# Performance work log

Hardware: AMD Instinct MI355X
Metric: run time of the kernel (lower is better)

The kernel has to match this reference:

```python
import jax, jax.numpy as jnp
import numpy as np

D_MODEL = 1024
N_HEADS = 16
D_K = D_MODEL // N_HEADS


def setup_inputs() -> dict:
    key = jax.random.key(0)
    ks = jax.random.split(key, 7)
    B, S = 2, 2048
    q = jax.random.normal(ks[0], (B, S, D_MODEL), dtype=jnp.float32)
    k = jax.random.normal(ks[1], (B, S, D_MODEL), dtype=jnp.float32)
    v = jax.random.normal(ks[2], (B, S, D_MODEL), dtype=jnp.float32)
    mask = jnp.ones((B, 1, S, S), dtype=bool)
    scale = 1.0 / np.sqrt(D_MODEL)
    w_q = jax.random.normal(ks[3], (D_MODEL, D_MODEL), dtype=jnp.float32) * scale
    w_k = jax.random.normal(ks[4], (D_MODEL, D_MODEL), dtype=jnp.float32) * scale
    w_v = jax.random.normal(ks[5], (D_MODEL, D_MODEL), dtype=jnp.float32) * scale
    w_o = jax.random.normal(ks[6], (D_MODEL, D_MODEL), dtype=jnp.float32) * scale
    return {"q": q, "k": k, "v": v, "mask": mask,
            "w_q": w_q, "w_k": w_k, "w_v": w_v, "w_o": w_o}


def reference(q, k, v, mask, w_q, w_k, w_v, w_o):
    B, S, _ = q.shape
    # projections (nn.Linear: x @ W^T, no bias)
    def split_heads(x):  # [B,S,D] -> [B,H,S,d_k]
        return x.reshape(B, -1, N_HEADS, D_K).transpose(0, 2, 1, 3)
    query = split_heads(q @ w_q.T)
    key_h = split_heads(k @ w_k.T)
    value = split_heads(v @ w_v.T)
    # naive scaled dot-product attention: full [B,H,S,S] scores materialized
    scores = jnp.einsum('bhqd,bhkd->bhqk', query, key_h) / jnp.sqrt(
        jnp.asarray(D_K, query.dtype))
    scores = jnp.where(mask, scores, jnp.asarray(-1e9, scores.dtype))
    attn = jax.nn.softmax(scores, axis=-1)  # dropout p=0.0 -> identity
    x = jnp.einsum('bhqk,bhkd->bhqd', attn, value)
    x = x.transpose(0, 2, 1, 3).reshape(B, S, N_HEADS * D_K)
    return x @ w_o.T
```

## Files before the change

kernel.cpp:

```cpp
#include <hip/hip_runtime.h>
#include <hip/hip_bf16.h>
#include <math.h>

typedef __bf16 bf16;
typedef __bf16 bf16x8 __attribute__((ext_vector_type(8)));
typedef float f32x4 __attribute__((ext_vector_type(4)));
typedef float f32x16 __attribute__((ext_vector_type(16)));
typedef unsigned u32x4 __attribute__((ext_vector_type(4)));

#define MFMA16(a, b, c) __builtin_amdgcn_mfma_f32_16x16x32_bf16((a), (b), (c), 0, 0, 0)
#define MFMA32(a, b, c) __builtin_amdgcn_mfma_f32_32x32x16_bf16((a), (b), (c), 0, 0, 0)

__device__ __forceinline__ void gl_lds16(const void* g, void* l) {
    __builtin_amdgcn_global_load_lds(
        (__attribute__((address_space(1))) void*)(g),
        (__attribute__((address_space(3))) void*)(l),
        16, 0, 0);
}

__device__ __forceinline__ unsigned cvt_pk_bf16(float lo, float hi) {
    unsigned r;
    asm("v_cvt_pk_bf16_f32 %0, %1, %2" : "=v"(r) : "v"(lo), "v"(hi));
    return r;
}

__global__ __launch_bounds__(256) void cvt7(
    const float* __restrict__ w0, const float* __restrict__ w1,
    const float* __restrict__ w2, const float* __restrict__ w3,
    const float* __restrict__ x0, const float* __restrict__ x1,
    const float* __restrict__ x2, bf16* __restrict__ dst) {
    const int z = blockIdx.y;
    const float* src;
    bf16* out;
    if (z < 4) {
        if (blockIdx.x >= 512) return;
        src = (z == 0) ? w0 : (z == 1) ? w1 : (z == 2) ? w2 : w3;
        out = dst + (size_t)z * 1048576;
    } else {
        src = (z == 4) ? x0 : (z == 5) ? x1 : x2;
        out = dst + 4 * 1048576 + (size_t)(z - 4) * 4194304;
    }
    const int i = (blockIdx.x * 256 + threadIdx.x) * 8;
    float4 a = ((const float4*)(src + i))[0];
    float4 b = ((const float4*)(src + i))[1];
    bf16x8 o;
    o[0] = (bf16)a.x; o[1] = (bf16)a.y; o[2] = (bf16)a.z; o[3] = (bf16)a.w;
    o[4] = (bf16)b.x; o[5] = (bf16)b.y; o[6] = (bf16)b.z; o[7] = (bf16)b.w;
    *(bf16x8*)(out + i) = o;
}

template <int EP>
__device__ __forceinline__ void gemm_bf(const bf16* __restrict__ A,
                                        const bf16* __restrict__ B,
                                        void* __restrict__ Cv,
                                        const int m0, const int n0) {
    constexpr int K = 1024;
    __shared__ __align__(16) bf16 As[128 * 64];
    __shared__ __align__(16) bf16 Bs[128 * 64];

    const int t = threadIdx.x;
    const int lane = t & 63;
    const int w = t >> 6;
    const int wm = (w & 1) * 64;
    const int wn = (w >> 1) * 64;
    const int lr = lane & 15;
    const int lq8 = (lane >> 4) * 8;
    const int rq = (lane >> 4) * 4;

    f32x4 acc[4][4] = {};

    const int srow = t >> 3;
    const int sch = (t & 7) * 8;
    char* lA = (char*)As;
    char* lB = (char*)Bs;

    for (int k0 = 0; k0 < K; k0 += 64) {
#pragma unroll
        for (int i = 0; i < 4; ++i) {
            gl_lds16(A + (size_t)(m0 + i * 32 + srow) * K + k0 + sch, lA + i * 4096 + t * 16);
            gl_lds16(B + (size_t)(n0 + i * 32 + srow) * K + k0 + sch, lB + i * 4096 + t * 16);
        }
        __syncthreads();

#pragma unroll
        for (int kk = 0; kk < 64; kk += 32) {
            bf16x8 af[4], bfr[4];
#pragma unroll
            for (int i = 0; i < 4; ++i) {
                af[i]  = *(const bf16x8*)&As[(wm + i * 16 + lr) * 64 + kk + lq8];
                bfr[i] = *(const bf16x8*)&Bs[(wn + i * 16 + lr) * 64 + kk + lq8];
            }
#pragma unroll
            for (int mi = 0; mi < 4; ++mi)
#pragma unroll
                for (int ni = 0; ni < 4; ++ni)
                    acc[mi][ni] = MFMA16(af[mi], bfr[ni], acc[mi][ni]);
        }
        __syncthreads();
    }

#pragma unroll
    for (int mi = 0; mi < 4; ++mi) {
#pragma unroll
        for (int ni = 0; ni < 4; ++ni) {
#pragma unroll
            for (int r = 0; r < 4; ++r) {
                const int m = m0 + wm + mi * 16 + rq + r;
                const int n = n0 + wn + ni * 16 + lr;
                const float vv = acc[mi][ni][r];
                if constexpr (EP == 0) {
                    bf16* C = (bf16*)Cv;
                    const int b = m >> 11, s = m & 2047;
                    const int h = n >> 6,  d = n & 63;
                    C[(((size_t)(b * 16 + h)) * 2048 + s) * 64 + d] = (bf16)vv;
                } else if constexpr (EP == 1) {
                    float* C = (float*)Cv;
                    C[(size_t)m * 1024 + n] = vv;
                } else {
                    bf16* C = (bf16*)Cv;
                    C[((size_t)(n >> 11) * 1024 + m) * 2048 + (n & 2047)] = (bf16)vv;
                }
            }
        }
    }
}

__global__ __launch_bounds__(256, 3) void qkv_bf(
    const bf16* __restrict__ Xq, const bf16* __restrict__ Xk,
    const bf16* __restrict__ Xv, const bf16* __restrict__ Wc,
    bf16* __restrict__ Qb, bf16* __restrict__ Kb, bf16* __restrict__ Vb) {
    const int z = blockIdx.z;
    if (z == 0)
        gemm_bf<0>(Xq, Wc, Qb, blockIdx.x * 128, blockIdx.y * 128);
    else if (z == 1)
        gemm_bf<0>(Xk, Wc + 1048576, Kb, blockIdx.x * 128, blockIdx.y * 128);
    else
        gemm_bf<2>(Wc + 2 * 1048576, Xv, Vb, blockIdx.y * 128, blockIdx.x * 128);
}

__global__ __launch_bounds__(512, 2) void out_gemm(
    const bf16* __restrict__ X, const bf16* __restrict__ W, float* __restrict__ C) {
    constexpr int K = 1024;
    __shared__ __align__(16) bf16 As[128 * 64];
    __shared__ __align__(16) bf16 Bs[128 * 64];

    const int t = threadIdx.x;
    const int lane = t & 63;
    const int w = t >> 6;
    const int wm = (w >> 2) * 64;
    const int wn = (w & 3) * 32;
    const int lr = lane & 15;
    const int lq8 = (lane >> 4) * 8;
    const int rq = (lane >> 4) * 4;
    const int m0 = blockIdx.x * 128, n0 = blockIdx.y * 128;

    f32x4 acc[4][2] = {};

    const int srow = t >> 3;
    const int sch = (t & 7) * 8;
    char* lA = (char*)As;
    char* lB = (char*)Bs;

    for (int k0 = 0; k0 < K; k0 += 64) {
#pragma unroll
        for (int i = 0; i < 2; ++i) {
            gl_lds16(X + (size_t)(m0 + i * 64 + srow) * K + k0 + sch, lA + i * 8192 + t * 16);
            gl_lds16(W + (size_t)(n0 + i * 64 + srow) * K + k0 + sch, lB + i * 8192 + t * 16);
        }
        __syncthreads();

#pragma unroll
        for (int kk = 0; kk < 64; kk += 32) {
            bf16x8 af[4], bfr[2];
#pragma unroll
            for (int i = 0; i < 4; ++i)
                af[i] = *(const bf16x8*)&As[(wm + i * 16 + lr) * 64 + kk + lq8];
#pragma unroll
            for (int i = 0; i < 2; ++i)
                bfr[i] = *(const bf16x8*)&Bs[(wn + i * 16 + lr) * 64 + kk + lq8];
#pragma unroll
            for (int mi = 0; mi < 4; ++mi)
#pragma unroll
                for (int ni = 0; ni < 2; ++ni)
                    acc[mi][ni] = MFMA16(af[mi], bfr[ni], acc[mi][ni]);
        }
        __syncthreads();
    }

#pragma unroll
    for (int mi = 0; mi < 4; ++mi)
#pragma unroll
        for (int ni = 0; ni < 2; ++ni)
#pragma unroll
            for (int r = 0; r < 4; ++r) {
                const int m = m0 + wm + mi * 16 + rq + r;
                const int n = n0 + wn + ni * 16 + lr;
                C[(size_t)m * 1024 + n] = acc[mi][ni][r];
            }
}

template <int MODE>
__device__ __forceinline__ void gemm_f32tok(const void* __restrict__ Av,
                                            const void* __restrict__ Bv,
                                            bf16* __restrict__ C,
                                            const int m0, const int n0) {
    constexpr int K = 1024;
    __shared__ __align__(16) bf16 As[128 * 32];
    __shared__ __align__(16) bf16 Bs[128 * 32];

    const int t = threadIdx.x;
    const int lane = t & 63;
    const int w = t >> 6;
    const int wm = (w & 1) * 64;
    const int wn = (w >> 1) * 64;
    const int lr = lane & 15;
    const int lq8 = (lane >> 4) * 8;
    const int rq = (lane >> 4) * 4;

    f32x4 acc[4][4] = {};
    const int srow = t >> 2;
    const int sch = (t & 3) * 8;
    const int ar = t >> 1;
    const int ac = (t & 1) * 16;
    char* lA = (char*)As;
    char* lB = (char*)Bs;

    for (int k0 = 0; k0 < K; k0 += 32) {
        if constexpr (MODE == 0) {
            const float* X = (const float*)Av;
            const float* p = X + (size_t)(m0 + ar) * K + k0 + ac;
            float4 f0 = ((const float4*)p)[0], f1 = ((const float4*)p)[1];
            float4 f2 = ((const float4*)p)[2], f3 = ((const float4*)p)[3];
            bf16x8 o0, o1;
            o0[0]=(bf16)f0.x; o0[1]=(bf16)f0.y; o0[2]=(bf16)f0.z; o0[3]=(bf16)f0.w;
            o0[4]=(bf16)f1.x; o0[5]=(bf16)f1.y; o0[6]=(bf16)f1.z; o0[7]=(bf16)f1.w;
            o1[0]=(bf16)f2.x; o1[1]=(bf16)f2.y; o1[2]=(bf16)f2.z; o1[3]=(bf16)f2.w;
            o1[4]=(bf16)f3.x; o1[5]=(bf16)f3.y; o1[6]=(bf16)f3.z; o1[7]=(bf16)f3.w;
            *(bf16x8*)&As[ar * 32 + ac]     = o0;
            *(bf16x8*)&As[ar * 32 + ac + 8] = o1;
        } else {
            const bf16* X = (const bf16*)Av;
            gl_lds16(X + (size_t)(m0 + srow) * K + k0 + sch,      lA + t * 16);
            gl_lds16(X + (size_t)(m0 + 64 + srow) * K + k0 + sch, lA + 4096 + t * 16);
        }
        if constexpr (MODE == 2) {
            const float* X = (const float*)Bv;
            const float* p = X + (size_t)(n0 + ar) * K + k0 + ac;
            float4 f0 = ((const float4*)p)[0], f1 = ((const float4*)p)[1];
            float4 f2 = ((const float4*)p)[2], f3 = ((const float4*)p)[3];
            bf16x8 o0, o1;
            o0[0]=(bf16)f0.x; o0[1]=(bf16)f0.y; o0[2]=(bf16)f0.z; o0[3]=(bf16)f0.w;
            o0[4]=(bf16)f1.x; o0[5]=(bf16)f1.y; o0[6]=(bf16)f1.z; o0[7]=(bf16)f1.w;
            o1[0]=(bf16)f2.x; o1[1]=(bf16)f2.y; o1[2]=(bf16)f2.z; o1[3]=(bf16)f2.w;
            o1[4]=(bf16)f3.x; o1[5]=(bf16)f3.y; o1[6]=(bf16)f3.z; o1[7]=(bf16)f3.w;
            *(bf16x8*)&Bs[ar * 32 + ac]     = o0;
            *(bf16x8*)&Bs[ar * 32 + ac + 8] = o1;
        } else {
            const bf16* W = (const bf16*)Bv;
            gl_lds16(W + (size_t)(n0 + srow) * K + k0 + sch,      lB + t * 16);
            gl_lds16(W + (size_t)(n0 + 64 + srow) * K + k0 + sch, lB + 4096 + t * 16);
        }
        __syncthreads();

        bf16x8 af[4], bfr[4];
#pragma unroll
        for (int i = 0; i < 4; ++i) {
            af[i]  = *(const bf16x8*)&As[(wm + i * 16 + lr) * 32 + lq8];
            bfr[i] = *(const bf16x8*)&Bs[(wn + i * 16 + lr) * 32 + lq8];
        }
#pragma unroll
        for (int mi = 0; mi < 4; ++mi)
#pragma unroll
            for (int ni = 0; ni < 4; ++ni)
                acc[mi][ni] = MFMA16(af[mi], bfr[ni], acc[mi][ni]);
        __syncthreads();
    }

#pragma unroll
    for (int mi = 0; mi < 4; ++mi) {
#pragma unroll
        for (int ni = 0; ni < 4; ++ni) {
#pragma unroll
            for (int r = 0; r < 4; ++r) {
                const int m = m0 + wm + mi * 16 + rq + r;
                const int n = n0 + wn + ni * 16 + lr;
                const float vv = acc[mi][ni][r];
                if constexpr (MODE == 0) {
                    const int b = m >> 11, s = m & 2047;
                    const int h = n >> 6,  d = n & 63;
                    C[(((size_t)(b * 16 + h)) * 2048 + s) * 64 + d] = (bf16)vv;
                } else {
                    C[((size_t)(n >> 11) * 1024 + m) * 2048 + (n & 2047)] = (bf16)vv;
                }
            }
        }
    }
}

__global__ __launch_bounds__(256, 2) void qkv_f32(
    const float* __restrict__ q, const float* __restrict__ k, const float* __restrict__ v,
    const bf16* __restrict__ Wc, bf16* __restrict__ Qb, bf16* __restrict__ Kb,
    bf16* __restrict__ Vb) {
    const int z = blockIdx.z;
    if (z == 0)
        gemm_f32tok<0>(q, Wc, Qb, blockIdx.x * 128, blockIdx.y * 128);
    else if (z == 1)
        gemm_f32tok<0>(k, Wc + 1048576, Kb, blockIdx.x * 128, blockIdx.y * 128);
    else
        gemm_f32tok<2>(Wc + 2 * 1048576, v, Vb, blockIdx.y * 128, blockIdx.x * 128);
}

__global__ __launch_bounds__(512, 4) void attn_kernel(
    const bf16* __restrict__ Qb, const bf16* __restrict__ Kb,
    const bf16* __restrict__ Vb, bf16* __restrict__ Xb) {
    constexpr int S = 2048;

    __shared__ __align__(16) bf16 smem[17408];

    const int t = threadIdx.x;
    const int lane = t & 63;
    const int w = t >> 6;
    const int wg = w & 3;
    const int kh = w >> 2;
    const int l31 = lane & 31;
    const int half = lane >> 5;

    const int lin = blockIdx.x;
    const int g = lin >> 3;
    const int bh = (lin & 7) + 8 * (g & 3);
    const int q0 = (g >> 2) * 128 + wg * 32;

    const bf16* Q  = Qb + (size_t)bh * S * 64;
    const bf16* Kh = Kb + (size_t)bh * S * 64;
    const bf16* Vh = Vb + (size_t)bh * 64 * S;

    const float qscale = 0.125f * 1.4426950408889634f;
    bf16x8 qf[4];
#pragma unroll
    for (int c = 0; c < 4; ++c) {
        bf16x8 v0 = *(const bf16x8*)(Q + (size_t)(q0 + l31) * 64 + c * 16 + half * 8);
#pragma unroll
        for (int e = 0; e < 8; ++e) v0[e] = (bf16)((float)v0[e] * qscale);
        qf[c] = v0;
    }

    f32x16 od[2] = {};
    float ls0 = 0.f, ls1 = 0.f, ls2 = 0.f, ls3 = 0.f;

    const int tt = t & 255;
    const int sr = tt >> 2;
    const int sc = (tt & 3) * 2;
    const bf16* pKg = Kh + ((size_t)kh * 1024 + sr) * 64 + sc * 8;
    const bf16* pVg = Vh + (size_t)sr * S + kh * 1024 + sc * 8;
    bf16* KsH = smem + kh * 4096;
    bf16* VsH = smem + 8192 + kh * 4096;
    int wKo[2];
#pragma unroll
    for (int c = 0; c < 2; ++c)
        wKo[c] = (sr >> 1) * 128 + ((((sr & 1) << 3) + sc + c) ^ ((sr >> 1) & 15)) * 8;

    bf16x8 pk[2], pv[2];
#pragma unroll
    for (int c = 0; c < 2; ++c) {
        pk[c] = *(const bf16x8*)(pKg + c * 8);
        pv[c] = *(const bf16x8*)(pVg + c * 8);
    }

    const int fbase = (l31 >> 1) * 128;
    const int fb8 = (l31 & 1) << 3;
    const int fsw = l31 >> 1;

    for (int j = 0; j < 16; ++j) {
        __syncthreads();
#pragma unroll
        for (int c = 0; c < 2; ++c) {
            *(bf16x8*)&KsH[wKo[c]] = pk[c];
            *(bf16x8*)&VsH[wKo[c]] = pv[c];
        }
        __syncthreads();

        f32x16 sacc[2] = {};
        __builtin_amdgcn_s_setprio(1);
#pragma unroll
        for (int kt = 0; kt < 2; ++kt) {
#pragma unroll
            for (int c = 0; c < 4; ++c) {
                bf16x8 kf = *(const bf16x8*)
                    &KsH[kt * 2048 + fbase + ((fb8 + c * 2 + half) ^ fsw) * 8];
                sacc[kt] = MFMA32(kf, qf[c], sacc[kt]);
            }
        }
        __builtin_amdgcn_s_setprio(0);

        if (j + 1 < 16) {
            pKg += 4096;
            pVg += 64;
#pragma unroll
            for (int c = 0; c < 2; ++c) {
                pk[c] = *(const bf16x8*)(pKg + c * 8);
                pv[c] = *(const bf16x8*)(pVg + c * 8);
            }
        }

#pragma unroll
        for (int kt = 0; kt < 2; ++kt) {
            float ex[16];
#pragma unroll
            for (int r = 0; r < 16; ++r)
                ex[r] = exp2f(sacc[kt][r]);
            ls0 += ex[0] + ex[4] + ex[8]  + ex[12];
            ls1 += ex[1] + ex[5] + ex[9]  + ex[13];
            ls2 += ex[2] + ex[6] + ex[10] + ex[14];
            ls3 += ex[3] + ex[7] + ex[11] + ex[15];

            unsigned pa[8];
#pragma unroll
            for (int c2 = 0; c2 < 2; ++c2) {
#pragma unroll
                for (int wd = 0; wd < 2; ++wd) {
                    unsigned x = cvt_pk_bf16(ex[c2 * 8 + wd * 2 + 0], ex[c2 * 8 + wd * 2 + 1]);
                    unsigned y = cvt_pk_bf16(ex[c2 * 8 + wd * 2 + 4], ex[c2 * 8 + wd * 2 + 5]);
                    asm("v_permlane32_swap_b32 %0, %1" : "+v"(x), "+v"(y));
                    pa[c2 * 4 + wd]     = x;
                    pa[c2 * 4 + wd + 2] = y;
                }
            }

            __builtin_amdgcn_s_setprio(1);
#pragma unroll
            for (int c2 = 0; c2 < 2; ++c2) {
                u32x4 aw;
                aw[0] = pa[c2 * 4 + 0]; aw[1] = pa[c2 * 4 + 1];
                aw[2] = pa[c2 * 4 + 2]; aw[3] = pa[c2 * 4 + 3];
                bf16x8 ap = __builtin_bit_cast(bf16x8, aw);
#pragma unroll
                for (int dt = 0; dt < 2; ++dt) {
                    const int cgv = kt * 4 + c2 * 2 + half;
                    bf16x8 vf = *(const bf16x8*)
                        &VsH[dt * 2048 + fbase + ((fb8 + cgv) ^ fsw) * 8];
                    od[dt] = MFMA32(ap, vf, od[dt]);
                }
            }
            __builtin_amdgcn_s_setprio(0);
        }
    }

    float lsum = ls0 + ls1 + ls2 + ls3;
    float ltot = lsum + __shfl_xor(lsum, 32);

    __syncthreads();
    float* fsm = (float*)smem;
    const int so = (wg * 64 + lane) * 34;
    if (kh == 1) {
        fsm[so + 32] = ltot;
#pragma unroll
        for (int r = 0; r < 16; ++r) {
            fsm[so + r]      = od[0][r];
            fsm[so + 16 + r] = od[1][r];
        }
    }
    __syncthreads();
    if (kh == 0) {
        ltot += fsm[so + 32];
        const float inv = 1.f / fmaxf(ltot, 1e-30f);
        const int b = bh >> 4, hh = bh & 15;
#pragma unroll
        for (int r = 0; r < 16; ++r) {
            const int qrow = (r & 3) + 8 * (r >> 2) + 4 * half;
            const float invr = __shfl(inv, qrow);
            const size_t base = ((size_t)(b * 2048 + q0 + qrow)) * 1024 + hh * 64;
            Xb[base + l31]      = (bf16)((od[0][r] + fsm[so + r]) * invr);
            Xb[base + 32 + l31] = (bf16)((od[1][r] + fsm[so + 16 + r]) * invr);
        }
    }
}

extern "C" void kernel_launch(void* const* d_in, const int* in_sizes, int n_in,
                              void* d_out, int out_size, void* d_ws, size_t ws_size,
                              hipStream_t stream) {
    const float* q  = (const float*)d_in[0];
    const float* k  = (const float*)d_in[1];
    const float* v  = (const float*)d_in[2];
    const float* wq = (const float*)d_in[4];
    const float* wk = (const float*)d_in[5];
    const float* wv = (const float*)d_in[6];
    const float* wo = (const float*)d_in[7];
    float* out = (float*)d_out;

    const bool big = ws_size >= (size_t)64 * 1024 * 1024;
    bf16* Wc = (bf16*)d_ws;
    const dim3 blk(256);

    if (big) {
        bf16* Xq = Wc + 4 * 1048576;
        bf16* Xk = Xq + 4194304;
        bf16* Xv = Xk + 4194304;
        bf16* Qb = Xv + 4194304;
        bf16* Kb = Qb + 4194304;
        bf16* Vb = Kb + 4194304;
        bf16* Xb = Vb + 4194304;
        cvt7<<<dim3(2048, 7), blk, 0, stream>>>(wq, wk, wv, wo, q, k, v, Wc);
        qkv_bf<<<dim3(32, 8, 3), blk, 0, stream>>>(Xq, Xk, Xv, Wc, Qb, Kb, Vb);
        attn_kernel<<<dim3(512), dim3(512), 0, stream>>>(Qb, Kb, Vb, Xb);
        out_gemm<<<dim3(32, 8), dim3(512), 0, stream>>>(Xb, Wc + 3 * 1048576, out);
    } else {
        bf16* Qb = Wc + 4 * 1048576;
        bf16* Kb = Qb + 4194304;
        bf16* Vb = Kb + 4194304;
        bf16* Xb = Vb + 4194304;
        cvt7<<<dim3(512, 4), blk, 0, stream>>>(wq, wk, wv, wo, q, k, v, Wc);
        qkv_f32<<<dim3(32, 8, 3), blk, 0, stream>>>(q, k, v, Wc, Qb, Kb, Vb);
        attn_kernel<<<dim3(512), dim3(512), 0, stream>>>(Qb, Kb, Vb, Xb);
        out_gemm<<<dim3(32, 8), dim3(512), 0, stream>>>(Xb, Wc + 3 * 1048576, out);
    }
}
```

Baseline: 267.6 us.

## Swizzle GEMM LDS tiles and give each attention wave two query tiles

The bf16 GEMM kernels now XOR-swizzle the 16-byte chunk index when staging tiles into LDS and when reading fragments, to avoid LDS bank conflicts on the MFMA operand loads. The attention kernel drops from 512 to 256 threads per block, with each wave handling 64 query rows (two 32-row tiles). Each K/V fragment read from LDS is therefore reused for two MFMAs, and each thread stages twice as many K/V chunks. The global prefetch of the next K/V tile now starts before the QK MFMAs, and the s_setprio hints are removed. This raises register pressure and halves waves per block, which can reduce latency hiding.

```diff
diff --git a/kernel.cpp b/kernel.cpp
--- a/kernel.cpp
+++ b/kernel.cpp
@@ -64,21 +64,22 @@
     const int wm = (w & 1) * 64;
     const int wn = (w >> 1) * 64;
     const int lr = lane & 15;
-    const int lq8 = (lane >> 4) * 8;
     const int rq = (lane >> 4) * 4;
+    const int ch0 = lane >> 4;
+    const int lsw = lr & 7;
 
     f32x4 acc[4][4] = {};
 
     const int srow = t >> 3;
-    const int sch = (t & 7) * 8;
+    const int scg = ((t & 7) ^ (srow & 7)) * 8;
     char* lA = (char*)As;
     char* lB = (char*)Bs;
 
     for (int k0 = 0; k0 < K; k0 += 64) {
 #pragma unroll
         for (int i = 0; i < 4; ++i) {
-            gl_lds16(A + (size_t)(m0 + i * 32 + srow) * K + k0 + sch, lA + i * 4096 + t * 16);
-            gl_lds16(B + (size_t)(n0 + i * 32 + srow) * K + k0 + sch, lB + i * 4096 + t * 16);
+            gl_lds16(A + (size_t)(m0 + i * 32 + srow) * K + k0 + scg, lA + i * 4096 + t * 16);
+            gl_lds16(B + (size_t)(n0 + i * 32 + srow) * K + k0 + scg, lB + i * 4096 + t * 16);
         }
         __syncthreads();
 
@@ -87,8 +88,10 @@
             bf16x8 af[4], bfr[4];
 #pragma unroll
             for (int i = 0; i < 4; ++i) {
-                af[i]  = *(const bf16x8*)&As[(wm + i * 16 + lr) * 64 + kk + lq8];
-                bfr[i] = *(const bf16x8*)&Bs[(wn + i * 16 + lr) * 64 + kk + lq8];
+                const int ro = (wm + i * 16 + lr) * 64 + ((((kk >> 3) + ch0) ^ lsw) * 8);
+                const int co = (wn + i * 16 + lr) * 64 + ((((kk >> 3) + ch0) ^ lsw) * 8);
+                af[i]  = *(const bf16x8*)&As[ro];
+                bfr[i] = *(const bf16x8*)&Bs[co];
             }
 #pragma unroll
             for (int mi = 0; mi < 4; ++mi)
@@ -150,22 +153,23 @@
     const int wm = (w >> 2) * 64;
     const int wn = (w & 3) * 32;
     const int lr = lane & 15;
-    const int lq8 = (lane >> 4) * 8;
     const int rq = (lane >> 4) * 4;
+    const int ch0 = lane >> 4;
+    const int lsw = lr & 7;
     const int m0 = blockIdx.x * 128, n0 = blockIdx.y * 128;
 
     f32x4 acc[4][2] = {};
 
     const int srow = t >> 3;
-    const int sch = (t & 7) * 8;
+    const int scg = ((t & 7) ^ (srow & 7)) * 8;
     char* lA = (char*)As;
     char* lB = (char*)Bs;
 
     for (int k0 = 0; k0 < K; k0 += 64) {
 #pragma unroll
         for (int i = 0; i < 2; ++i) {
-            gl_lds16(X + (size_t)(m0 + i * 64 + srow) * K + k0 + sch, lA + i * 8192 + t * 16);
-            gl_lds16(W + (size_t)(n0 + i * 64 + srow) * K + k0 + sch, lB + i * 8192 + t * 16);
+            gl_lds16(X + (size_t)(m0 + i * 64 + srow) * K + k0 + scg, lA + i * 8192 + t * 16);
+            gl_lds16(W + (size_t)(n0 + i * 64 + srow) * K + k0 + scg, lB + i * 8192 + t * 16);
         }
         __syncthreads();
 
@@ -174,10 +178,10 @@
             bf16x8 af[4], bfr[2];
 #pragma unroll
             for (int i = 0; i < 4; ++i)
-                af[i] = *(const bf16x8*)&As[(wm + i * 16 + lr) * 64 + kk + lq8];
+                af[i] = *(const bf16x8*)&As[(wm + i * 16 + lr) * 64 + ((((kk >> 3) + ch0) ^ lsw) * 8)];
 #pragma unroll
             for (int i = 0; i < 2; ++i)
-                bfr[i] = *(const bf16x8*)&Bs[(wn + i * 16 + lr) * 64 + kk + lq8];
+                bfr[i] = *(const bf16x8*)&Bs[(wn + i * 16 + lr) * 64 + ((((kk >> 3) + ch0) ^ lsw) * 8)];
 #pragma unroll
             for (int mi = 0; mi < 4; ++mi)
 #pragma unroll
@@ -310,7 +314,7 @@
         gemm_f32tok<2>(Wc + 2 * 1048576, v, Vb, blockIdx.y * 128, blockIdx.x * 128);
 }
 
-__global__ __launch_bounds__(512, 4) void attn_kernel(
+__global__ __launch_bounds__(256, 2) void attn_kernel(
     const bf16* __restrict__ Qb, const bf16* __restrict__ Kb,
     const bf16* __restrict__ Vb, bf16* __restrict__ Xb) {
     constexpr int S = 2048;
@@ -320,48 +324,53 @@
     const int t = threadIdx.x;
     const int lane = t & 63;
     const int w = t >> 6;
-    const int wg = w & 3;
-    const int kh = w >> 2;
+    const int wg = w & 1;
+    const int kh = w >> 1;
     const int l31 = lane & 31;
     const int half = lane >> 5;
 
     const int lin = blockIdx.x;
     const int g = lin >> 3;
     const int bh = (lin & 7) + 8 * (g & 3);
-    const int q0 = (g >> 2) * 128 + wg * 32;
+    const int q0 = (g >> 2) * 128 + wg * 64;
 
     const bf16* Q  = Qb + (size_t)bh * S * 64;
     const bf16* Kh = Kb + (size_t)bh * S * 64;
     const bf16* Vh = Vb + (size_t)bh * 64 * S;
 
     const float qscale = 0.125f * 1.4426950408889634f;
-    bf16x8 qf[4];
+    bf16x8 qfA[4], qfB[4];
 #pragma unroll
     for (int c = 0; c < 4; ++c) {
         bf16x8 v0 = *(const bf16x8*)(Q + (size_t)(q0 + l31) * 64 + c * 16 + half * 8);
-#pragma unroll
-        for (int e = 0; e < 8; ++e) v0[e] = (bf16)((float)v0[e] * qscale);
-        qf[c] = v0;
-    }
-
-    f32x16 od[2] = {};
-    float ls0 = 0.f, ls1 = 0.f, ls2 = 0.f, ls3 = 0.f;
-
-    const int tt = t & 255;
-    const int sr = tt >> 2;
-    const int sc = (tt & 3) * 2;
-    const bf16* pKg = Kh + ((size_t)kh * 1024 + sr) * 64 + sc * 8;
-    const bf16* pVg = Vh + (size_t)sr * S + kh * 1024 + sc * 8;
+        bf16x8 v1 = *(const bf16x8*)(Q + (size_t)(q0 + 32 + l31) * 64 + c * 16 + half * 8);
+#pragma unroll
+        for (int e = 0; e < 8; ++e) {
+            v0[e] = (bf16)((float)v0[e] * qscale);
+            v1[e] = (bf16)((float)v1[e] * qscale);
+        }
+        qfA[c] = v0;
+        qfB[c] = v1;
+    }
+
+    f32x16 odA[2] = {}, odB[2] = {};
+    float lsA0 = 0.f, lsA1 = 0.f, lsB0 = 0.f, lsB1 = 0.f;
+
+    const int tt = t & 127;
+    const int sr = tt >> 1;
+    const int scb = (tt & 1) * 4;
+    const bf16* pKg = Kh + ((size_t)kh * 1024 + sr) * 64 + scb * 8;
+    const bf16* pVg = Vh + (size_t)sr * S + kh * 1024 + scb * 8;
     bf16* KsH = smem + kh * 4096;
     bf16* VsH = smem + 8192 + kh * 4096;
-    int wKo[2];
-#pragma unroll
-    for (int c = 0; c < 2; ++c)
-        wKo[c] = (sr >> 1) * 128 + ((((sr & 1) << 3) + sc + c) ^ ((sr >> 1) & 15)) * 8;
-
-    bf16x8 pk[2], pv[2];
-#pragma unroll
-    for (int c = 0; c < 2; ++c) {
+    int wKo[4];
+#pragma unroll
+    for (int c = 0; c < 4; ++c)
+        wKo[c] = (sr >> 1) * 128 + ((((sr & 1) << 3) + scb + c) ^ ((sr >> 1) & 15)) * 8;
+
+    bf16x8 pk[4], pv[4];
+#pragma unroll
+    for (int c = 0; c < 4; ++c) {
         pk[c] = *(const bf16x8*)(pKg + c * 8);
         pv[c] = *(const bf16x8*)(pVg + c * 8);
     }
@@ -373,104 +382,120 @@
     for (int j = 0; j < 16; ++j) {
         __syncthreads();
 #pragma unroll
-        for (int c = 0; c < 2; ++c) {
+        for (int c = 0; c < 4; ++c) {
             *(bf16x8*)&KsH[wKo[c]] = pk[c];
             *(bf16x8*)&VsH[wKo[c]] = pv[c];
         }
         __syncthreads();
 
-        f32x16 sacc[2] = {};
-        __builtin_amdgcn_s_setprio(1);
+        if (j + 1 < 16) {
+            pKg += 4096;
+            pVg += 64;
+#pragma unroll
+            for (int c = 0; c < 4; ++c) {
+                pk[c] = *(const bf16x8*)(pKg + c * 8);
+                pv[c] = *(const bf16x8*)(pVg + c * 8);
+            }
+        }
+
 #pragma unroll
         for (int kt = 0; kt < 2; ++kt) {
+            f32x16 sA = {}, sB = {};
 #pragma unroll
             for (int c = 0; c < 4; ++c) {
                 bf16x8 kf = *(const bf16x8*)
                     &KsH[kt * 2048 + fbase + ((fb8 + c * 2 + half) ^ fsw) * 8];
-                sacc[kt] = MFMA32(kf, qf[c], sacc[kt]);
-            }
-        }
-        __builtin_amdgcn_s_setprio(0);
-
-        if (j + 1 < 16) {
-            pKg += 4096;
-            pVg += 64;
-#pragma unroll
-            for (int c = 0; c < 2; ++c) {
-                pk[c] = *(const bf16x8*)(pKg + c * 8);
-                pv[c] = *(const bf16x8*)(pVg + c * 8);
-            }
-        }
-
-#pragma unroll
-        for (int kt = 0; kt < 2; ++kt) {
-            float ex[16];
-#pragma unroll
-            for (int r = 0; r < 16; ++r)
-                ex[r] = exp2f(sacc[kt][r]);
-            ls0 += ex[0] + ex[4] + ex[8]  + ex[12];
-            ls1 += ex[1] + ex[5] + ex[9]  + ex[13];
-            ls2 += ex[2] + ex[6] + ex[10] + ex[14];
-            ls3 += ex[3] + ex[7] + ex[11] + ex[15];
-
-            unsigned pa[8];
+                sA = MFMA32(kf, qfA[c], sA);
+                sB = MFMA32(kf, qfB[c], sB);
+            }
+
+            float exA[16], exB[16];
+#pragma unroll
+            for (int r = 0; r < 16; ++r) {
+                exA[r] = exp2f(sA[r]);
+                exB[r] = exp2f(sB[r]);
+            }
+            lsA0 += exA[0] + exA[4] + exA[8]  + exA[12] + exA[2] + exA[6] + exA[10] + exA[14];
+            lsA1 += exA[1] + exA[5] + exA[9]  + exA[13] + exA[3] + exA[7] + exA[11] + exA[15];
+            lsB0 += exB[0] + exB[4] + exB[8]  + exB[12] + exB[2] + exB[6] + exB[10] + exB[14];
+            lsB1 += exB[1] + exB[5] + exB[9]  + exB[13] + exB[3] + exB[7] + exB[11] + exB[15];
+
+            unsigned paA[8], paB[8];
 #pragma unroll
             for (int c2 = 0; c2 < 2; ++c2) {
 #pragma unroll
                 for (int wd = 0; wd < 2; ++wd) {
-                    unsigned x = cvt_pk_bf16(ex[c2 * 8 + wd * 2 + 0], ex[c2 * 8 + wd * 2 + 1]);
-                    unsigned y = cvt_pk_bf16(ex[c2 * 8 + wd * 2 + 4], ex[c2 * 8 + wd * 2 + 5]);
-                    asm("v_permlane32_swap_b32 %0, %1" : "+v"(x), "+v"(y));
-                    pa[c2 * 4 + wd]     = x;
-                    pa[c2 * 4 + wd + 2] = y;
+                    unsigned xa = cvt_pk_bf16(exA[c2 * 8 + wd * 2 + 0], exA[c2 * 8 + wd * 2 + 1]);
+                    unsigned ya = cvt_pk_bf16(exA[c2 * 8 + wd * 2 + 4], exA[c2 * 8 + wd * 2 + 5]);
+                    asm("v_permlane32_swap_b32 %0, %1" : "+v"(xa), "+v"(ya));
+                    paA[c2 * 4 + wd]     = xa;
+                    paA[c2 * 4 + wd + 2] = ya;
+                    unsigned xb = cvt_pk_bf16(exB[c2 * 8 + wd * 2 + 0], exB[c2 * 8 + wd * 2 + 1]);
+                    unsigned yb = cvt_pk_bf16(exB[c2 * 8 + wd * 2 + 4], exB[c2 * 8 + wd * 2 + 5]);
+                    asm("v_permlane32_swap_b32 %0, %1" : "+v"(xb), "+v"(yb));
+                    paB[c2 * 4 + wd]     = xb;
+                    paB[c2 * 4 + wd + 2] = yb;
                 }
             }
 
-            __builtin_amdgcn_s_setprio(1);
 #pragma unroll
             for (int c2 = 0; c2 < 2; ++c2) {
-                u32x4 aw;
-                aw[0] = pa[c2 * 4 + 0]; aw[1] = pa[c2 * 4 + 1];
-                aw[2] = pa[c2 * 4 + 2]; aw[3] = pa[c2 * 4 + 3];
-                bf16x8 ap = __builtin_bit_cast(bf16x8, aw);
+                u32x4 awA, awB;
+                awA[0] = paA[c2 * 4 + 0]; awA[1] = paA[c2 * 4 + 1];
+                awA[2] = paA[c2 * 4 + 2]; awA[3] = paA[c2 * 4 + 3];
+                awB[0] = paB[c2 * 4 + 0]; awB[1] = paB[c2 * 4 + 1];
+                awB[2] = paB[c2 * 4 + 2]; awB[3] = paB[c2 * 4 + 3];
+                bf16x8 apA = __builtin_bit_cast(bf16x8, awA);
+                bf16x8 apB = __builtin_bit_cast(bf16x8, awB);
 #pragma unroll
                 for (int dt = 0; dt < 2; ++dt) {
                     const int cgv = kt * 4 + c2 * 2 + half;
                     bf16x8 vf = *(const bf16x8*)
                         &VsH[dt * 2048 + fbase + ((fb8 + cgv) ^ fsw) * 8];
-                    od[dt] = MFMA32(ap, vf, od[dt]);
+                    odA[dt] = MFMA32(apA, vf, odA[dt]);
+                    odB[dt] = MFMA32(apB, vf, odB[dt]);
                 }
             }
-            __builtin_amdgcn_s_setprio(0);
-        }
-    }
-
-    float lsum = ls0 + ls1 + ls2 + ls3;
-    float ltot = lsum + __shfl_xor(lsum, 32);
+        }
+    }
+
+    float lsumA = lsA0 + lsA1;
+    float lsumB = lsB0 + lsB1;
+    float ltotA = lsumA + __shfl_xor(lsumA, 32);
+    float ltotB = lsumB + __shfl_xor(lsumB, 32);
 
     __syncthreads();
     float* fsm = (float*)smem;
-    const int so = (wg * 64 + lane) * 34;
+    const int so = (wg * 64 + lane) * 66;
     if (kh == 1) {
-        fsm[so + 32] = ltot;
+        fsm[so + 64] = ltotA;
+        fsm[so + 65] = ltotB;
 #pragma unroll
         for (int r = 0; r < 16; ++r) {
-            fsm[so + r]      = od[0][r];
-            fsm[so + 16 + r] = od[1][r];
+            fsm[so + r]      = odA[0][r];
+            fsm[so + 16 + r] = odA[1][r];
+            fsm[so + 32 + r] = odB[0][r];
+            fsm[so + 48 + r] = odB[1][r];
         }
     }
     __syncthreads();
     if (kh == 0) {
-        ltot += fsm[so + 32];
-        const float inv = 1.f / fmaxf(ltot, 1e-30f);
+        ltotA += fsm[so + 64];
+        ltotB += fsm[so + 65];
+        const float invA = 1.f / fmaxf(ltotA, 1e-30f);
+        const float invB = 1.f / fmaxf(ltotB, 1e-30f);
         const int b = bh >> 4, hh = bh & 15;
 #pragma unroll
         for (int r = 0; r < 16; ++r) {
             const int qrow = (r & 3) + 8 * (r >> 2) + 4 * half;
-            const float invr = __shfl(inv, qrow);
-            const size_t base = ((size_t)(b * 2048 + q0 + qrow)) * 1024 + hh * 64;
-            Xb[base + l31]      = (bf16)((od[0][r] + fsm[so + r]) * invr);
-            Xb[base + 32 + l31] = (bf16)((od[1][r] + fsm[so + 16 + r]) * invr);
+            const float invAr = __shfl(invA, qrow);
+            const float invBr = __shfl(invB, qrow);
+            const size_t baseA = ((size_t)(b * 2048 + q0 + qrow)) * 1024 + hh * 64;
+            const size_t baseB = ((size_t)(b * 2048 + q0 + 32 + qrow)) * 1024 + hh * 64;
+            Xb[baseA + l31]      = (bf16)((odA[0][r] + fsm[so + r])      * invAr);
+            Xb[baseA + 32 + l31] = (bf16)((odA[1][r] + fsm[so + 16 + r]) * invAr);
+            Xb[baseB + l31]      = (bf16)((odB[0][r] + fsm[so + 32 + r]) * invBr);
+            Xb[baseB + 32 + l31] = (bf16)((odB[1][r] + fsm[so + 48 + r]) * invBr);
         }
     }
 }
@@ -501,7 +526,7 @@
         bf16* Xb = Vb + 4194304;
         cvt7<<<dim3(2048, 7), blk, 0, stream>>>(wq, wk, wv, wo, q, k, v, Wc);
         qkv_bf<<<dim3(32, 8, 3), blk, 0, stream>>>(Xq, Xk, Xv, Wc, Qb, Kb, Vb);
-        attn_kernel<<<dim3(512), dim3(512), 0, stream>>>(Qb, Kb, Vb, Xb);
+        attn_kernel<<<dim3(512), dim3(256), 0, stream>>>(Qb, Kb, Vb, Xb);
         out_gemm<<<dim3(32, 8), dim3(512), 0, stream>>>(Xb, Wc + 3 * 1048576, out);
     } else {
         bf16* Qb = Wc + 4 * 1048576;
@@ -510,7 +535,7 @@
         bf16* Xb = Vb + 4194304;
         cvt7<<<dim3(512, 4), blk, 0, stream>>>(wq, wk, wv, wo, q, k, v, Wc);
         qkv_f32<<<dim3(32, 8, 3), blk, 0, stream>>>(q, k, v, Wc, Qb, Kb, Vb);
-        attn_kernel<<<dim3(512), dim3(512), 0, stream>>>(Qb, Kb, Vb, Xb);
+        attn_kernel<<<dim3(512), dim3(256), 0, stream>>>(Qb, Kb, Vb, Xb);
         out_gemm<<<dim3(32, 8), dim3(512), 0, stream>>>(Xb, Wc + 3 * 1048576, out);
     }
 }
```

Result: faster. 243.1 us (-9.2%).

## Halve attention block size, interleave QK per tile, XOR-swizzle GEMM LDS tiles

Applied to the files above, without the earlier changes.

The attention kernel moves from 512-thread blocks covering 128 query rows to 256-thread blocks covering 64 rows, launched as 1024 blocks instead of 512. Each thread now stages four K/V chunks instead of two. The QK^T MFMAs are computed per key tile right before their exp/PV use rather than all up front, and the setprio hints are dropped. The QKV and output GEMMs gain an XOR swizzle on their LDS layout to cut bank conflicts on fragment reads. The gains are meant to come from finer-grained scheduling and less register pressure, at the cost of more K/V reloads per query row and less QK/PV overlap.

```diff
diff --git a/kernel.cpp b/kernel.cpp
--- a/kernel.cpp
+++ b/kernel.cpp
@@ -64,21 +64,22 @@
     const int wm = (w & 1) * 64;
     const int wn = (w >> 1) * 64;
     const int lr = lane & 15;
-    const int lq8 = (lane >> 4) * 8;
     const int rq = (lane >> 4) * 4;
+    const int ch0 = lane >> 4;
+    const int lsw = lr & 7;
 
     f32x4 acc[4][4] = {};
 
     const int srow = t >> 3;
-    const int sch = (t & 7) * 8;
+    const int scg = ((t & 7) ^ (srow & 7)) * 8;
     char* lA = (char*)As;
     char* lB = (char*)Bs;
 
     for (int k0 = 0; k0 < K; k0 += 64) {
 #pragma unroll
         for (int i = 0; i < 4; ++i) {
-            gl_lds16(A + (size_t)(m0 + i * 32 + srow) * K + k0 + sch, lA + i * 4096 + t * 16);
-            gl_lds16(B + (size_t)(n0 + i * 32 + srow) * K + k0 + sch, lB + i * 4096 + t * 16);
+            gl_lds16(A + (size_t)(m0 + i * 32 + srow) * K + k0 + scg, lA + i * 4096 + t * 16);
+            gl_lds16(B + (size_t)(n0 + i * 32 + srow) * K + k0 + scg, lB + i * 4096 + t * 16);
         }
         __syncthreads();
 
@@ -87,8 +88,10 @@
             bf16x8 af[4], bfr[4];
 #pragma unroll
             for (int i = 0; i < 4; ++i) {
-                af[i]  = *(const bf16x8*)&As[(wm + i * 16 + lr) * 64 + kk + lq8];
-                bfr[i] = *(const bf16x8*)&Bs[(wn + i * 16 + lr) * 64 + kk + lq8];
+                const int ro = (wm + i * 16 + lr) * 64 + ((((kk >> 3) + ch0) ^ lsw) * 8);
+                const int co = (wn + i * 16 + lr) * 64 + ((((kk >> 3) + ch0) ^ lsw) * 8);
+                af[i]  = *(const bf16x8*)&As[ro];
+                bfr[i] = *(const bf16x8*)&Bs[co];
             }
 #pragma unroll
             for (int mi = 0; mi < 4; ++mi)
@@ -150,22 +153,23 @@
     const int wm = (w >> 2) * 64;
     const int wn = (w & 3) * 32;
     const int lr = lane & 15;
-    const int lq8 = (lane >> 4) * 8;
     const int rq = (lane >> 4) * 4;
+    const int ch0 = lane >> 4;
+    const int lsw = lr & 7;
     const int m0 = blockIdx.x * 128, n0 = blockIdx.y * 128;
 
     f32x4 acc[4][2] = {};
 
     const int srow = t >> 3;
-    const int sch = (t & 7) * 8;
+    const int scg = ((t & 7) ^ (srow & 7)) * 8;
     char* lA = (char*)As;
     char* lB = (char*)Bs;
 
     for (int k0 = 0; k0 < K; k0 += 64) {
 #pragma unroll
         for (int i = 0; i < 2; ++i) {
-            gl_lds16(X + (size_t)(m0 + i * 64 + srow) * K + k0 + sch, lA + i * 8192 + t * 16);
-            gl_lds16(W + (size_t)(n0 + i * 64 + srow) * K + k0 + sch, lB + i * 8192 + t * 16);
+            gl_lds16(X + (size_t)(m0 + i * 64 + srow) * K + k0 + scg, lA + i * 8192 + t * 16);
+            gl_lds16(W + (size_t)(n0 + i * 64 + srow) * K + k0 + scg, lB + i * 8192 + t * 16);
         }
         __syncthreads();
 
@@ -174,10 +178,10 @@
             bf16x8 af[4], bfr[2];
 #pragma unroll
             for (int i = 0; i < 4; ++i)
-                af[i] = *(const bf16x8*)&As[(wm + i * 16 + lr) * 64 + kk + lq8];
+                af[i] = *(const bf16x8*)&As[(wm + i * 16 + lr) * 64 + ((((kk >> 3) + ch0) ^ lsw) * 8)];
 #pragma unroll
             for (int i = 0; i < 2; ++i)
-                bfr[i] = *(const bf16x8*)&Bs[(wn + i * 16 + lr) * 64 + kk + lq8];
+                bfr[i] = *(const bf16x8*)&Bs[(wn + i * 16 + lr) * 64 + ((((kk >> 3) + ch0) ^ lsw) * 8)];
 #pragma unroll
             for (int mi = 0; mi < 4; ++mi)
 #pragma unroll
@@ -310,7 +314,7 @@
         gemm_f32tok<2>(Wc + 2 * 1048576, v, Vb, blockIdx.y * 128, blockIdx.x * 128);
 }
 
-__global__ __launch_bounds__(512, 4) void attn_kernel(
+__global__ __launch_bounds__(256, 4) void attn_kernel(
     const bf16* __restrict__ Qb, const bf16* __restrict__ Kb,
     const bf16* __restrict__ Vb, bf16* __restrict__ Xb) {
     constexpr int S = 2048;
@@ -320,15 +324,15 @@
     const int t = threadIdx.x;
     const int lane = t & 63;
     const int w = t >> 6;
-    const int wg = w & 3;
-    const int kh = w >> 2;
+    const int wg = w & 1;
+    const int kh = w >> 1;
     const int l31 = lane & 31;
     const int half = lane >> 5;
 
     const int lin = blockIdx.x;
     const int g = lin >> 3;
     const int bh = (lin & 7) + 8 * (g & 3);
-    const int q0 = (g >> 2) * 128 + wg * 32;
+    const int q0 = (g >> 2) * 64 + wg * 32;
 
     const bf16* Q  = Qb + (size_t)bh * S * 64;
     const bf16* Kh = Kb + (size_t)bh * S * 64;
@@ -347,21 +351,21 @@
     f32x16 od[2] = {};
     float ls0 = 0.f, ls1 = 0.f, ls2 = 0.f, ls3 = 0.f;
 
-    const int tt = t & 255;
-    const int sr = tt >> 2;
-    const int sc = (tt & 3) * 2;
-    const bf16* pKg = Kh + ((size_t)kh * 1024 + sr) * 64 + sc * 8;
-    const bf16* pVg = Vh + (size_t)sr * S + kh * 1024 + sc * 8;
+    const int tt = t & 127;
+    const int sr = tt >> 1;
+    const int scb = (tt & 1) * 4;
+    const bf16* pKg = Kh + ((size_t)kh * 1024 + sr) * 64 + scb * 8;
+    const bf16* pVg = Vh + (size_t)sr * S + kh * 1024 + scb * 8;
     bf16* KsH = smem + kh * 4096;
     bf16* VsH = smem + 8192 + kh * 4096;
-    int wKo[2];
-#pragma unroll
-    for (int c = 0; c < 2; ++c)
-        wKo[c] = (sr >> 1) * 128 + ((((sr & 1) << 3) + sc + c) ^ ((sr >> 1) & 15)) * 8;
-
-    bf16x8 pk[2], pv[2];
-#pragma unroll
-    for (int c = 0; c < 2; ++c) {
+    int wKo[4];
+#pragma unroll
+    for (int c = 0; c < 4; ++c)
+        wKo[c] = (sr >> 1) * 128 + ((((sr & 1) << 3) + scb + c) ^ ((sr >> 1) & 15)) * 8;
+
+    bf16x8 pk[4], pv[4];
+#pragma unroll
+    for (int c = 0; c < 4; ++c) {
         pk[c] = *(const bf16x8*)(pKg + c * 8);
         pv[c] = *(const bf16x8*)(pVg + c * 8);
     }
@@ -370,33 +374,22 @@
     const int fb8 = (l31 & 1) << 3;
     const int fsw = l31 >> 1;
 
+    const f32x16 fz = {};
+
     for (int j = 0; j < 16; ++j) {
         __syncthreads();
 #pragma unroll
-        for (int c = 0; c < 2; ++c) {
+        for (int c = 0; c < 4; ++c) {
             *(bf16x8*)&KsH[wKo[c]] = pk[c];
             *(bf16x8*)&VsH[wKo[c]] = pv[c];
         }
         __syncthreads();
-
-        f32x16 sacc[2] = {};
-        __builtin_amdgcn_s_setprio(1);
-#pragma unroll
-        for (int kt = 0; kt < 2; ++kt) {
-#pragma unroll
-            for (int c = 0; c < 4; ++c) {
-                bf16x8 kf = *(const bf16x8*)
-                    &KsH[kt * 2048 + fbase + ((fb8 + c * 2 + half) ^ fsw) * 8];
-                sacc[kt] = MFMA32(kf, qf[c], sacc[kt]);
-            }
-        }
-        __builtin_amdgcn_s_setprio(0);
 
         if (j + 1 < 16) {
             pKg += 4096;
             pVg += 64;
 #pragma unroll
-            for (int c = 0; c < 2; ++c) {
+            for (int c = 0; c < 4; ++c) {
                 pk[c] = *(const bf16x8*)(pKg + c * 8);
                 pv[c] = *(const bf16x8*)(pVg + c * 8);
             }
@@ -404,10 +397,20 @@
 
 #pragma unroll
         for (int kt = 0; kt < 2; ++kt) {
+            bf16x8 kf[4];
+#pragma unroll
+            for (int c = 0; c < 4; ++c)
+                kf[c] = *(const bf16x8*)
+                    &KsH[kt * 2048 + fbase + ((fb8 + c * 2 + half) ^ fsw) * 8];
+            f32x16 s = MFMA32(kf[0], qf[0], fz);
+#pragma unroll
+            for (int c = 1; c < 4; ++c)
+                s = MFMA32(kf[c], qf[c], s);
+
             float ex[16];
 #pragma unroll
             for (int r = 0; r < 16; ++r)
-                ex[r] = exp2f(sacc[kt][r]);
+                ex[r] = exp2f(s[r]);
             ls0 += ex[0] + ex[4] + ex[8]  + ex[12];
             ls1 += ex[1] + ex[5] + ex[9]  + ex[13];
             ls2 += ex[2] + ex[6] + ex[10] + ex[14];
@@ -426,7 +429,6 @@
                 }
             }
 
-            __builtin_amdgcn_s_setprio(1);
 #pragma unroll
             for (int c2 = 0; c2 < 2; ++c2) {
                 u32x4 aw;
@@ -441,7 +443,6 @@
                     od[dt] = MFMA32(ap, vf, od[dt]);
                 }
             }
-            __builtin_amdgcn_s_setprio(0);
         }
     }
 
@@ -450,7 +451,7 @@
 
     __syncthreads();
     float* fsm = (float*)smem;
-    const int so = (wg * 64 + lane) * 34;
+    const int so = (wg * 64 + lane) * 33;
     if (kh == 1) {
         fsm[so + 32] = ltot;
 #pragma unroll
@@ -501,7 +502,7 @@
         bf16* Xb = Vb + 4194304;
         cvt7<<<dim3(2048, 7), blk, 0, stream>>>(wq, wk, wv, wo, q, k, v, Wc);
         qkv_bf<<<dim3(32, 8, 3), blk, 0, stream>>>(Xq, Xk, Xv, Wc, Qb, Kb, Vb);
-        attn_kernel<<<dim3(512), dim3(512), 0, stream>>>(Qb, Kb, Vb, Xb);
+        attn_kernel<<<dim3(1024), dim3(256), 0, stream>>>(Qb, Kb, Vb, Xb);
         out_gemm<<<dim3(32, 8), dim3(512), 0, stream>>>(Xb, Wc + 3 * 1048576, out);
     } else {
         bf16* Qb = Wc + 4 * 1048576;
@@ -510,7 +511,7 @@
         bf16* Xb = Vb + 4194304;
         cvt7<<<dim3(512, 4), blk, 0, stream>>>(wq, wk, wv, wo, q, k, v, Wc);
         qkv_f32<<<dim3(32, 8, 3), blk, 0, stream>>>(q, k, v, Wc, Qb, Kb, Vb);
-        attn_kernel<<<dim3(512), dim3(512), 0, stream>>>(Qb, Kb, Vb, Xb);
+        attn_kernel<<<dim3(1024), dim3(256), 0, stream>>>(Qb, Kb, Vb, Xb);
         out_gemm<<<dim3(32, 8), dim3(512), 0, stream>>>(Xb, Wc + 3 * 1048576, out);
     }
 }
```

Result: faster. 250.4 us (-6.4%).

## Double-buffer LDS tiles in QKV and output GEMMs; drop setprio in attention

Applied to the files above, without the earlier changes.

The QKV and output-projection GEMMs now use two LDS buffers with a K-step of 32, prefetching the next tile via global_load_lds while MFMAs run on the current one. This is meant to hide global-to-LDS latency and remove one barrier per iteration, at the cost of twice as many loop iterations and smaller MFMA batches between barriers. Separately, the s_setprio raise/lower pairs around the attention MFMA sections are removed, which changes wave scheduling priority in the attention kernel.

```diff
diff --git a/kernel.cpp b/kernel.cpp
--- a/kernel.cpp
+++ b/kernel.cpp
@@ -55,8 +55,8 @@
                                         void* __restrict__ Cv,
                                         const int m0, const int n0) {
     constexpr int K = 1024;
-    __shared__ __align__(16) bf16 As[128 * 64];
-    __shared__ __align__(16) bf16 Bs[128 * 64];
+    __shared__ __align__(16) bf16 As[2][128 * 32];
+    __shared__ __align__(16) bf16 Bs[2][128 * 32];
 
     const int t = threadIdx.x;
     const int lane = t & 63;
@@ -69,35 +69,46 @@
 
     f32x4 acc[4][4] = {};
 
-    const int srow = t >> 3;
-    const int sch = (t & 7) * 8;
+    const int srow = t >> 2;
+    const int sch = (t & 3) * 8;
     char* lA = (char*)As;
     char* lB = (char*)Bs;
 
-    for (int k0 = 0; k0 < K; k0 += 64) {
+#define QSTAGE(buf, k0)                                                              \
+    do {                                                                             \
+        gl_lds16(A + (size_t)(m0 + srow) * K + (k0) + sch,                           \
+                 lA + (buf) * 8192 + t * 16);                                        \
+        gl_lds16(A + (size_t)(m0 + 64 + srow) * K + (k0) + sch,                      \
+                 lA + (buf) * 8192 + 4096 + t * 16);                                 \
+        gl_lds16(B + (size_t)(n0 + srow) * K + (k0) + sch,                           \
+                 lB + (buf) * 8192 + t * 16);                                        \
+        gl_lds16(B + (size_t)(n0 + 64 + srow) * K + (k0) + sch,                      \
+                 lB + (buf) * 8192 + 4096 + t * 16);                                 \
+    } while (0)
+
+    QSTAGE(0, 0);
+    __syncthreads();
+
+    int cur = 0;
+    for (int k0 = 0; k0 < K; k0 += 32) {
+        if (k0 + 32 < K) QSTAGE(cur ^ 1, k0 + 32);
+
+        bf16x8 af[4], bfr[4];
 #pragma unroll
         for (int i = 0; i < 4; ++i) {
-            gl_lds16(A + (size_t)(m0 + i * 32 + srow) * K + k0 + sch, lA + i * 4096 + t * 16);
-            gl_lds16(B + (size_t)(n0 + i * 32 + srow) * K + k0 + sch, lB + i * 4096 + t * 16);
-        }
+            af[i]  = *(const bf16x8*)&As[cur][(wm + i * 16 + lr) * 32 + lq8];
+            bfr[i] = *(const bf16x8*)&Bs[cur][(wn + i * 16 + lr) * 32 + lq8];
+        }
+#pragma unroll
+        for (int mi = 0; mi < 4; ++mi)
+#pragma unroll
+            for (int ni = 0; ni < 4; ++ni)
+                acc[mi][ni] = MFMA16(af[mi], bfr[ni], acc[mi][ni]);
+
         __syncthreads();
-
-#pragma unroll
-        for (int kk = 0; kk < 64; kk += 32) {
-            bf16x8 af[4], bfr[4];
-#pragma unroll
-            for (int i = 0; i < 4; ++i) {
-                af[i]  = *(const bf16x8*)&As[(wm + i * 16 + lr) * 64 + kk + lq8];
-                bfr[i] = *(const bf16x8*)&Bs[(wn + i * 16 + lr) * 64 + kk + lq8];
-            }
-#pragma unroll
-            for (int mi = 0; mi < 4; ++mi)
-#pragma unroll
-                for (int ni = 0; ni < 4; ++ni)
-                    acc[mi][ni] = MFMA16(af[mi], bfr[ni], acc[mi][ni]);
-        }
-        __syncthreads();
-    }
+        cur ^= 1;
+    }
+#undef QSTAGE
 
 #pragma unroll
     for (int mi = 0; mi < 4; ++mi) {
@@ -141,8 +152,8 @@
 __global__ __launch_bounds__(512, 2) void out_gemm(
     const bf16* __restrict__ X, const bf16* __restrict__ W, float* __restrict__ C) {
     constexpr int K = 1024;
-    __shared__ __align__(16) bf16 As[128 * 64];
-    __shared__ __align__(16) bf16 Bs[128 * 64];
+    __shared__ __align__(16) bf16 As[2][128 * 32];
+    __shared__ __align__(16) bf16 Bs[2][128 * 32];
 
     const int t = threadIdx.x;
     const int lane = t & 63;
@@ -156,36 +167,43 @@
 
     f32x4 acc[4][2] = {};
 
-    const int srow = t >> 3;
-    const int sch = (t & 7) * 8;
+    const int srow = t >> 2;
+    const int sch = (t & 3) * 8;
     char* lA = (char*)As;
     char* lB = (char*)Bs;
 
-    for (int k0 = 0; k0 < K; k0 += 64) {
-#pragma unroll
-        for (int i = 0; i < 2; ++i) {
-            gl_lds16(X + (size_t)(m0 + i * 64 + srow) * K + k0 + sch, lA + i * 8192 + t * 16);
-            gl_lds16(W + (size_t)(n0 + i * 64 + srow) * K + k0 + sch, lB + i * 8192 + t * 16);
-        }
+#define OSTAGE(buf, k0)                                                              \
+    do {                                                                             \
+        gl_lds16(X + (size_t)(m0 + srow) * K + (k0) + sch,                           \
+                 lA + (buf) * 8192 + t * 16);                                        \
+        gl_lds16(W + (size_t)(n0 + srow) * K + (k0) + sch,                           \
+                 lB + (buf) * 8192 + t * 16);                                        \
+    } while (0)
+
+    OSTAGE(0, 0);
+    __syncthreads();
+
+    int cur = 0;
+    for (int k0 = 0; k0 < K; k0 += 32) {
+        if (k0 + 32 < K) OSTAGE(cur ^ 1, k0 + 32);
+
+        bf16x8 af[4], bfr[2];
+#pragma unroll
+        for (int i = 0; i < 4; ++i)
+            af[i] = *(const bf16x8*)&As[cur][(wm + i * 16 + lr) * 32 + lq8];
+#pragma unroll
+        for (int i = 0; i < 2; ++i)
+            bfr[i] = *(const bf16x8*)&Bs[cur][(wn + i * 16 + lr) * 32 + lq8];
+#pragma unroll
+        for (int mi = 0; mi < 4; ++mi)
+#pragma unroll
+            for (int ni = 0; ni < 2; ++ni)
+                acc[mi][ni] = MFMA16(af[mi], bfr[ni], acc[mi][ni]);
+
         __syncthreads();
-
-#pragma unroll
-        for (int kk = 0; kk < 64; kk += 32) {
-            bf16x8 af[4], bfr[2];
-#pragma unroll
-            for (int i = 0; i < 4; ++i)
-                af[i] = *(const bf16x8*)&As[(wm + i * 16 + lr) * 64 + kk + lq8];
-#pragma unroll
-            for (int i = 0; i < 2; ++i)
-                bfr[i] = *(const bf16x8*)&Bs[(wn + i * 16 + lr) * 64 + kk + lq8];
-#pragma unroll
-            for (int mi = 0; mi < 4; ++mi)
-#pragma unroll
-                for (int ni = 0; ni < 2; ++ni)
-                    acc[mi][ni] = MFMA16(af[mi], bfr[ni], acc[mi][ni]);
-        }
-        __syncthreads();
-    }
+        cur ^= 1;
+    }
+#undef OSTAGE
 
 #pragma unroll
     for (int mi = 0; mi < 4; ++mi)
@@ -380,7 +398,6 @@
         __syncthreads();
 
         f32x16 sacc[2] = {};
-        __builtin_amdgcn_s_setprio(1);
 #pragma unroll
         for (int kt = 0; kt < 2; ++kt) {
 #pragma unroll
@@ -390,7 +407,6 @@
                 sacc[kt] = MFMA32(kf, qf[c], sacc[kt]);
             }
         }
-        __builtin_amdgcn_s_setprio(0);
 
         if (j + 1 < 16) {
             pKg += 4096;
@@ -426,7 +442,6 @@
                 }
             }
 
-            __builtin_amdgcn_s_setprio(1);
 #pragma unroll
             for (int c2 = 0; c2 < 2; ++c2) {
                 u32x4 aw;
@@ -441,7 +456,6 @@
                     od[dt] = MFMA32(ap, vf, od[dt]);
                 }
             }
-            __builtin_amdgcn_s_setprio(0);
         }
     }
 
```

Result: faster. 243.4 us (-9.0%).
